# Performance work log

Measured on AMD Instinct MI355X. Metric: run time of the kernel, lower is better.

## Reference

```python
import jax, jax.numpy as jnp
import numpy as np

SCALING = 32.0 / 16.0  # alpha / r


def setup_inputs() -> dict:
    key = jax.random.key(0)
    k1, k2, k3, k4, k5 = jax.random.split(key, 5)
    B_, S, D_in, D_out, R = 4, 4096, 4096, 4096, 16
    x = jax.random.normal(k1, (B_, S, D_in), dtype=jnp.float32)
    W = jax.random.normal(k2, (D_in, D_out), dtype=jnp.float32) * 0.02
    b = jax.random.normal(k3, (D_out,), dtype=jnp.float32) * 0.02
    A = jax.random.normal(k4, (D_in, R), dtype=jnp.float32) * 0.02
    Bm = jax.random.normal(k5, (R, D_out), dtype=jnp.float32) * 0.02
    return {"x": x, "W": W, "b": b, "A": A, "B": Bm}


def reference(x, W, b, A, B):
    # base linear: y = x @ W + b  (torch Linear with weight W^T)
    base = jnp.einsum("bsd,de->bse", x, W) + b
    # low-rank update: x @ A @ B (associativity-exploiting; same math as x @ (A@B))
    lora = jnp.einsum("bsd,dr->bsr", x, A)
    lora = jnp.einsum("bsr,re->bse", lora, B)
    return base + lora * SCALING
```

## Files before the change

kernel.cpp:

```cpp
#include <hip/hip_runtime.h>

#define SCALE_LORA 2.0f
#define BM 256
#define BN 256
#define BKI 128

#define AS1 __attribute__((address_space(1)))
#define AS3 __attribute__((address_space(3)))

using f32x4  = __attribute__((ext_vector_type(4))) float;
using i32x4  = __attribute__((ext_vector_type(4))) int;
using i32x16 = __attribute__((ext_vector_type(16))) int;
using u16x8  = __attribute__((ext_vector_type(8))) unsigned short;

#define MFMAI8(a, b, c) __builtin_amdgcn_mfma_i32_32x32x32_i8((a), (b), (c), 0, 0, 0)

static __device__ __forceinline__ unsigned short f2bf_rne(float f) {
  unsigned int u = __builtin_bit_cast(unsigned int, f);
  u += 0x7FFFu + ((u >> 16) & 1u);
  return (unsigned short)(u >> 16);
}
static __device__ __forceinline__ float bf2f(unsigned short b) {
  unsigned int u = (unsigned int)b << 16;
  return __builtin_bit_cast(float, u);
}

__global__ void quant_x_kernel(const float* __restrict__ x,
                               signed char* __restrict__ xq,
                               float* __restrict__ sx, int K) {
  __shared__ float wmax[4];
  long row = blockIdx.x;
  const float* xr = x + row * (long)K;
  int t = threadIdx.x;
  f32x4 v[4];
  #pragma unroll
  for (int j = 0; j < 4; ++j)
    v[j] = *(const f32x4*)(xr + 4 * t + 1024 * j);
  float m = 0.f;
  #pragma unroll
  for (int j = 0; j < 4; ++j)
    #pragma unroll
    for (int e = 0; e < 4; ++e) m = fmaxf(m, fabsf(v[j][e]));
  #pragma unroll
  for (int off = 1; off < 64; off <<= 1)
    m = fmaxf(m, __shfl_xor(m, off));
  if ((t & 63) == 0) wmax[t >> 6] = m;
  __syncthreads();
  float rm = fmaxf(fmaxf(wmax[0], wmax[1]), fmaxf(wmax[2], wmax[3]));
  rm = fmaxf(rm, 1e-20f);
  float inv = 127.0f / rm;
  #pragma unroll
  for (int j = 0; j < 4; ++j) {
    int b0 = max(-127, min(127, (int)rintf(v[j][0] * inv)));
    int b1 = max(-127, min(127, (int)rintf(v[j][1] * inv)));
    int b2 = max(-127, min(127, (int)rintf(v[j][2] * inv)));
    int b3 = max(-127, min(127, (int)rintf(v[j][3] * inv)));
    unsigned int pk = (b0 & 255) | ((b1 & 255) << 8) | ((b2 & 255) << 16)
                      | ((unsigned)b3 << 24);
    *(unsigned int*)(xq + row * (long)K + 4 * t + 1024 * j) = pk;
  }
  if (t == 0) sx[row] = rm * (1.0f / 127.0f);
}

__global__ void build_wt_kernel(const float* __restrict__ W,
                                const float* __restrict__ A,
                                const float* __restrict__ Bmat,
                                unsigned short* __restrict__ WT,
                                int K, int N, int R) {
  __shared__ float Bs[16][64];
  __shared__ unsigned short Tt[64][66];
  int ntn = N >> 6;
  int kt = blockIdx.x / ntn, nt = blockIdx.x - kt * ntn;
  int k0 = kt << 6, n0 = nt << 6;
  int t = threadIdx.x;
  int tx = t & 63, ty = t >> 6;

  for (int i = t; i < R * 64; i += 256)
    Bs[i >> 6][i & 63] = Bmat[(long)(i >> 6) * N + n0 + (i & 63)];
  __syncthreads();

  for (int it = 0; it < 16; ++it) {
    int kl = (it << 2) + ty;
    long kg = k0 + kl;
    float w = W[kg * N + n0 + tx];
    const float* Ar = A + kg * R;
    float s = 0.f;
    for (int r = 0; r < R; ++r) s += Ar[r] * Bs[r][tx];
    Tt[kl][tx] = f2bf_rne(w + SCALE_LORA * s);
  }
  __syncthreads();

  for (int it = 0; it < 16; ++it) {
    int nn = (it << 2) + ty;
    WT[(long)(n0 + nn) * K + k0 + tx] = Tt[tx][nn];
  }
}

__global__ void quantize_wt_kernel(const unsigned short* __restrict__ WT,
                                   signed char* __restrict__ WTq,
                                   float* __restrict__ sw, int K) {
  __shared__ float wmax[4];
  long n = blockIdx.x;
  const unsigned short* wr = WT + n * (long)K;
  int t = threadIdx.x;
  u16x8 u0 = *(const u16x8*)(wr + 8 * t);
  u16x8 u1 = *(const u16x8*)(wr + 8 * t + 2048);
  float f0[8], f1[8];
  float m = 0.f;
  #pragma unroll
  for (int e = 0; e < 8; ++e) {
    f0[e] = bf2f(u0[e]); f1[e] = bf2f(u1[e]);
    m = fmaxf(m, fmaxf(fabsf(f0[e]), fabsf(f1[e])));
  }
  #pragma unroll
  for (int off = 1; off < 64; off <<= 1)
    m = fmaxf(m, __shfl_xor(m, off));
  if ((t & 63) == 0) wmax[t >> 6] = m;
  __syncthreads();
  float rm = fmaxf(fmaxf(wmax[0], wmax[1]), fmaxf(wmax[2], wmax[3]));
  rm = fmaxf(rm, 1e-20f);
  float inv = 127.0f / rm;
  unsigned long long p0 = 0, p1 = 0;
  #pragma unroll
  for (int e = 0; e < 8; ++e) {
    int q0 = max(-127, min(127, (int)rintf(f0[e] * inv)));
    int q1 = max(-127, min(127, (int)rintf(f1[e] * inv)));
    p0 |= (unsigned long long)(q0 & 255) << (8 * e);
    p1 |= (unsigned long long)(q1 & 255) << (8 * e);
  }
  *(unsigned long long*)(WTq + n * (long)K + 8 * t) = p0;
  *(unsigned long long*)(WTq + n * (long)K + 8 * t + 2048) = p1;
  if (t == 0) sw[n] = rm * (1.0f / 127.0f);
}

__global__ __launch_bounds__(512, 2) void gemm_kernel(
    const signed char* __restrict__ Xq,
    const signed char* __restrict__ WTq,
    const float* __restrict__ bias,
    const float* __restrict__ sx,
    const float* __restrict__ sw,
    float* __restrict__ out,
    int M, int N, int K)
{
  extern __shared__ char ldsc[];

  int nwg = gridDim.x;
  int bid = blockIdx.x;
  if ((nwg & 7) == 0) {
    int cpx = nwg >> 3;
    bid = (bid & 7) * cpx + (bid >> 3);
  }
  int ntn = N / BN;
  int tm = bid / ntn;
  int tn = bid - tm * ntn;
  const long m0 = (long)tm * BM;
  const long n0 = (long)tn * BN;

  int tid  = threadIdx.x;
  int lane = tid & 63;
  int wave = tid >> 6;
  int wr = wave >> 2;
  int wc = wave & 3;
  int l31 = lane & 31;
  int g   = lane >> 5;

  i32x16 acc[4][2] = {};

  int srcg = 16 * ((tid & 7) ^ ((tid >> 3) & 7));
  const signed char* aSrc = Xq + (m0 + (tid >> 3)) * (long)K + srcg;
  const signed char* bSrc = WTq + (n0 + (tid >> 3)) * (long)K + srcg;
  const int ldsByte = tid * 16;

  const int sw7 = l31 & 7;
  const int so0 = 16 * ((0 + g) ^ sw7);
  const int so1 = 16 * ((2 + g) ^ sw7);
  const int so2 = 16 * ((4 + g) ^ sw7);
  const int so3 = 16 * ((6 + g) ^ sw7);
  const int rowA = wr * 16384 + l31 * 128;
  const int rowB = wc * 8192  + l31 * 128;

  const int nt = K / BKI;

#define STGA(b, h, kt) do {                                                  \
    _Pragma("unroll")                                                        \
    for (int j_ = 0; j_ < 2; ++j_)                                           \
      __builtin_amdgcn_global_load_lds(                                      \
        (const AS1 void*)(aSrc + ((h)*128 + j_*64)*(long)K + (long)(kt)*BKI),\
        (AS3 void*)(ldsc + (b)*32768 + (h)*16384 + j_*8192 + ldsByte),       \
        16, 0, 0);                                                           \
  } while (0)
#define STGB(b, h, kt) do {                                                  \
    _Pragma("unroll")                                                        \
    for (int j_ = 0; j_ < 2; ++j_)                                           \
      __builtin_amdgcn_global_load_lds(                                      \
        (const AS1 void*)(bSrc + ((h)*128 + j_*64)*(long)K + (long)(kt)*BKI),\
        (AS3 void*)(ldsc + 65536 + (b)*32768 + (h)*16384 + j_*8192 +         \
                    ldsByte), 16, 0, 0);                                     \
  } while (0)

#define SBAR  __builtin_amdgcn_sched_barrier(0)
#define BAR   __builtin_amdgcn_s_barrier()
#define LGKM0 do { asm volatile("s_waitcnt lgkmcnt(0)" ::: "memory"); SBAR; } while (0)
#define LGKM8 do { asm volatile("s_waitcnt lgkmcnt(8)" ::: "memory"); } while (0)

#define RD_A(arr, fmB) do {                                                  \
    _Pragma("unroll")                                                        \
    for (int fi_ = 0; fi_ < 2; ++fi_) {                                      \
      const char* p_ = Ab_ + ((fmB) + fi_) * 4096;                           \
      arr[fi_][0] = *(const i32x4*)(p_ + so0);                               \
      arr[fi_][1] = *(const i32x4*)(p_ + so1);                               \
      arr[fi_][2] = *(const i32x4*)(p_ + so2);                               \
      arr[fi_][3] = *(const i32x4*)(p_ + so3);                               \
    }                                                                        \
  } while (0)
#define RD_B(arr, fnB) do {                                                  \
    const char* p_ = Bb_ + (fnB) * 4096;                                     \
    arr[0] = *(const i32x4*)(p_ + so0);                                      \
    arr[1] = *(const i32x4*)(p_ + so1);                                      \
    arr[2] = *(const i32x4*)(p_ + so2);                                      \
    arr[3] = *(const i32x4*)(p_ + so3);                                      \
  } while (0)
#define QUAD(aarr, barr, fmB, fn) do {                                       \
    __builtin_amdgcn_s_setprio(1);                                           \
    _Pragma("unroll")                                                        \
    for (int fi_ = 0; fi_ < 2; ++fi_)                                        \
      _Pragma("unroll")                                                      \
      for (int ks_ = 0; ks_ < 4; ++ks_)                                      \
        acc[(fmB)+fi_][fn] = MFMAI8(aarr[fi_][ks_], barr[ks_],               \
                                    acc[(fmB)+fi_][fn]);                     \
    __builtin_amdgcn_s_setprio(0);                                           \
  } while (0)

#define TILE4(B_, W1, S1, S2, S3, S4) do {                                   \
    asm volatile("s_waitcnt vmcnt(" W1 ")" ::: "memory");                    \
    BAR;                                                                     \
    const char* Ab_ = ldsc + (B_)*32768 + rowA;                              \
    const char* Bb_ = ldsc + 65536 + (B_)*32768 + rowB;                      \
    i32x4 af_[2][4], bl_[4], bh_[4], ag_[2][4];                              \
    RD_A(af_, 0);                                                            \
    RD_B(bl_, 0);                                                            \
    S1;                                                                      \
    LGKM8;                                                                   \
    SBAR; BAR; LGKM0;                                                        \
    QUAD(af_, bl_, 0, 0);                                                    \
    SBAR; BAR;                                                               \
    RD_B(bh_, 1);                                                            \
    S2;                                                                      \
    SBAR; BAR; LGKM0;                                                        \
    QUAD(af_, bh_, 0, 1);                                                    \
    SBAR; BAR;                                                               \
    RD_A(ag_, 2);                                                            \
    S3;                                                                      \
    SBAR; BAR; LGKM0;                                                        \
    QUAD(ag_, bl_, 2, 0);                                                    \
    SBAR; BAR;                                                               \
    S4;                                                                      \
    SBAR;                                                                    \
    QUAD(ag_, bh_, 2, 1);                                                    \
    SBAR;                                                                    \
  } while (0)

  STGB(0, 0, 0); STGA(0, 0, 0); STGB(0, 1, 0); STGA(0, 1, 0);
  STGB(1, 0, 1); STGA(1, 0, 1);

  const int npair = nt / 2;
  for (int i = 0; i < npair - 1; ++i) {
    int t2 = 2 * i;
    TILE4(0, "4", STGB(1,1,t2+1), STGA(1,1,t2+1), STGB(0,0,t2+2), STGA(0,0,t2+2));
    TILE4(1, "4", STGB(0,1,t2+2), STGA(0,1,t2+2), STGB(1,0,t2+3), STGA(1,0,t2+3));
  }
  TILE4(0, "4", STGB(1,1,nt-1), STGA(1,1,nt-1), , );
  TILE4(1, "0", , , , );

#undef TILE4
#undef QUAD
#undef RD_A
#undef RD_B
#undef STGA
#undef STGB

  #pragma unroll
  for (int fn = 0; fn < 2; ++fn) {
    long col = n0 + wc * 64 + fn * 32 + l31;
    float swc = sw[col];
    float bv = bias[col];
    #pragma unroll
    for (int fm = 0; fm < 4; ++fm) {
      long rbase = m0 + wr * 128 + fm * 32 + 4 * g;
      #pragma unroll
      for (int r = 0; r < 16; ++r) {
        long row = rbase + (r & 3) + 8 * (r >> 2);
        out[row * (long)N + col] = (float)acc[fm][fn][r] * sx[row] * swc + bv;
      }
    }
  }
}

extern "C" void kernel_launch(void* const* d_in, const int* in_sizes, int n_in,
                              void* d_out, int out_size, void* d_ws, size_t ws_size,
                              hipStream_t stream) {
  const float* x    = (const float*)d_in[0];
  const float* W    = (const float*)d_in[1];
  const float* b    = (const float*)d_in[2];
  const float* A    = (const float*)d_in[3];
  const float* Bm   = (const float*)d_in[4];

  const long D_out = in_sizes[2];
  const long D_in  = (long)in_sizes[1] / D_out;
  const long M     = (long)in_sizes[0] / D_in;
  const int  R     = (int)((long)in_sizes[3] / D_in);
  const int  K = (int)D_in, N = (int)D_out;

  char* wsc = (char*)d_ws;
  signed char*    xq  = (signed char*)wsc;
  unsigned short* wt  = (unsigned short*)(wsc + (size_t)M * K);
  signed char*    wtq = (signed char*)(wsc + (size_t)M * K + (size_t)N * K * 2);
  float* sx = (float*)(wsc + (size_t)M * K + (size_t)N * K * 3);
  float* sw = (float*)(wsc + (size_t)M * K + (size_t)N * K * 3 + (size_t)M * 4);

  quant_x_kernel<<<(int)M, 256, 0, stream>>>(x, xq, sx, K);
  build_wt_kernel<<<(K >> 6) * (N >> 6), 256, 0, stream>>>(W, A, Bm, wt, K, N, R);
  quantize_wt_kernel<<<N, 256, 0, stream>>>(wt, wtq, sw, K);

  int grid = (int)((M / BM) * ((long)N / BN));
  gemm_kernel<<<grid, 512, 128 * 1024, stream>>>(
      xq, wtq, b, sx, sw, (float*)d_out, (int)M, N, K);
}
```

Baseline: 446.3 us.

## Switch int8 GEMM main loop to 4-stage BK=64 pipeline with single barrier

Replaces the two-buffer, half-tile staged loop at K-step 128, which used many intra-tile barriers, with a four-buffer ring at K-step 64. Loads run three tiles ahead and each tile needs only one barrier. The LDS swizzle and row strides change to match the 64-byte rows. The aim is to cut barrier and synchronization overhead and to deepen prefetch. In exchange, the work per iteration halves and the bank-conflict behaviour of the new swizzle may differ.

```diff
diff --git a/kernel.cpp b/kernel.cpp
--- a/kernel.cpp
+++ b/kernel.cpp
@@ -3,7 +3,7 @@
 #define SCALE_LORA 2.0f
 #define BM 256
 #define BN 256
-#define BKI 128
+#define BKI 64
 
 #define AS1 __attribute__((address_space(1)))
 #define AS3 __attribute__((address_space(3)))
@@ -166,118 +166,92 @@
 
   i32x16 acc[4][2] = {};
 
-  int srcg = 16 * ((tid & 7) ^ ((tid >> 3) & 7));
-  const signed char* aSrc = Xq + (m0 + (tid >> 3)) * (long)K + srcg;
-  const signed char* bSrc = WTq + (n0 + (tid >> 3)) * (long)K + srcg;
+  int srccol = 16 * ((tid & 3) ^ ((tid >> 3) & 3));
+  const signed char* aSrc = Xq + (m0 + (tid >> 2)) * (long)K + srccol;
+  const signed char* bSrc = WTq + (n0 + (tid >> 2)) * (long)K + srccol;
   const int ldsByte = tid * 16;
 
-  const int sw7 = l31 & 7;
-  const int so0 = 16 * ((0 + g) ^ sw7);
-  const int so1 = 16 * ((2 + g) ^ sw7);
-  const int so2 = 16 * ((4 + g) ^ sw7);
-  const int so3 = 16 * ((6 + g) ^ sw7);
-  const int rowA = wr * 16384 + l31 * 128;
-  const int rowB = wc * 8192  + l31 * 128;
+  const int rsw = (l31 >> 1) & 3;
+  const int so0 = 16 * ((0 + g) ^ rsw);
+  const int so1 = 16 * ((2 + g) ^ rsw);
+  const int rowA = wr * 8192 + l31 * 64;
+  const int rowB = wc * 4096 + l31 * 64;
 
   const int nt = K / BKI;
 
-#define STGA(b, h, kt) do {                                                  \
+#define STAGEA(buf, kt) do {                                                 \
     _Pragma("unroll")                                                        \
     for (int j_ = 0; j_ < 2; ++j_)                                           \
       __builtin_amdgcn_global_load_lds(                                      \
-        (const AS1 void*)(aSrc + ((h)*128 + j_*64)*(long)K + (long)(kt)*BKI),\
-        (AS3 void*)(ldsc + (b)*32768 + (h)*16384 + j_*8192 + ldsByte),       \
+        (const AS1 void*)(aSrc + j_*128*(long)K + (long)(kt)*BKI),           \
+        (AS3 void*)(ldsc + (buf)*16384 + j_*8192 + ldsByte), 16, 0, 0);      \
+  } while (0)
+#define STAGEB(buf, kt) do {                                                 \
+    _Pragma("unroll")                                                        \
+    for (int j_ = 0; j_ < 2; ++j_)                                           \
+      __builtin_amdgcn_global_load_lds(                                      \
+        (const AS1 void*)(bSrc + j_*128*(long)K + (long)(kt)*BKI),           \
+        (AS3 void*)(ldsc + 65536 + (buf)*16384 + j_*8192 + ldsByte),         \
         16, 0, 0);                                                           \
   } while (0)
-#define STGB(b, h, kt) do {                                                  \
-    _Pragma("unroll")                                                        \
-    for (int j_ = 0; j_ < 2; ++j_)                                           \
-      __builtin_amdgcn_global_load_lds(                                      \
-        (const AS1 void*)(bSrc + ((h)*128 + j_*64)*(long)K + (long)(kt)*BKI),\
-        (AS3 void*)(ldsc + 65536 + (b)*32768 + (h)*16384 + j_*8192 +         \
-                    ldsByte), 16, 0, 0);                                     \
+
+#define SBAR  __builtin_amdgcn_sched_barrier(0)
+
+#define TILE(BUFI, VMSTR, STA, STB) do {                                     \
+    asm volatile("s_waitcnt vmcnt(" VMSTR ")" ::: "memory");                 \
+    __builtin_amdgcn_s_barrier();                                            \
+    SBAR;                                                                    \
+    const char* Ab_ = ldsc + (BUFI)*16384 + rowA;                            \
+    const char* Bb_ = ldsc + 65536 + (BUFI)*16384 + rowB;                    \
+    i32x4 a0_[4], a1_[4], b0_[2], b1_[2];                                    \
+    _Pragma("unroll")                                                        \
+    for (int fm_ = 0; fm_ < 4; ++fm_)                                        \
+      a0_[fm_] = *(const i32x4*)(Ab_ + fm_*2048 + so0);                      \
+    _Pragma("unroll")                                                        \
+    for (int fn_ = 0; fn_ < 2; ++fn_)                                        \
+      b0_[fn_] = *(const i32x4*)(Bb_ + fn_*2048 + so0);                      \
+    STA;                                                                     \
+    SBAR;                                                                    \
+    _Pragma("unroll")                                                        \
+    for (int fm_ = 0; fm_ < 4; ++fm_)                                        \
+      a1_[fm_] = *(const i32x4*)(Ab_ + fm_*2048 + so1);                      \
+    _Pragma("unroll")                                                        \
+    for (int fn_ = 0; fn_ < 2; ++fn_)                                        \
+      b1_[fn_] = *(const i32x4*)(Bb_ + fn_*2048 + so1);                      \
+    STB;                                                                     \
+    SBAR;                                                                    \
+    __builtin_amdgcn_s_setprio(1);                                           \
+    _Pragma("unroll")                                                        \
+    for (int fm_ = 0; fm_ < 4; ++fm_)                                        \
+      _Pragma("unroll")                                                      \
+      for (int fn_ = 0; fn_ < 2; ++fn_)                                      \
+        acc[fm_][fn_] = MFMAI8(a0_[fm_], b0_[fn_], acc[fm_][fn_]);           \
+    __builtin_amdgcn_s_setprio(0);                                           \
+    SBAR;                                                                    \
+    __builtin_amdgcn_s_setprio(1);                                           \
+    _Pragma("unroll")                                                        \
+    for (int fm_ = 0; fm_ < 4; ++fm_)                                        \
+      _Pragma("unroll")                                                      \
+      for (int fn_ = 0; fn_ < 2; ++fn_)                                      \
+        acc[fm_][fn_] = MFMAI8(a1_[fm_], b1_[fn_], acc[fm_][fn_]);           \
+    __builtin_amdgcn_s_setprio(0);                                           \
+    SBAR;                                                                    \
   } while (0)
 
-#define SBAR  __builtin_amdgcn_sched_barrier(0)
-#define BAR   __builtin_amdgcn_s_barrier()
-#define LGKM0 do { asm volatile("s_waitcnt lgkmcnt(0)" ::: "memory"); SBAR; } while (0)
-#define LGKM8 do { asm volatile("s_waitcnt lgkmcnt(8)" ::: "memory"); } while (0)
-
-#define RD_A(arr, fmB) do {                                                  \
-    _Pragma("unroll")                                                        \
-    for (int fi_ = 0; fi_ < 2; ++fi_) {                                      \
-      const char* p_ = Ab_ + ((fmB) + fi_) * 4096;                           \
-      arr[fi_][0] = *(const i32x4*)(p_ + so0);                               \
-      arr[fi_][1] = *(const i32x4*)(p_ + so1);                               \
-      arr[fi_][2] = *(const i32x4*)(p_ + so2);                               \
-      arr[fi_][3] = *(const i32x4*)(p_ + so3);                               \
-    }                                                                        \
-  } while (0)
-#define RD_B(arr, fnB) do {                                                  \
-    const char* p_ = Bb_ + (fnB) * 4096;                                     \
-    arr[0] = *(const i32x4*)(p_ + so0);                                      \
-    arr[1] = *(const i32x4*)(p_ + so1);                                      \
-    arr[2] = *(const i32x4*)(p_ + so2);                                      \
-    arr[3] = *(const i32x4*)(p_ + so3);                                      \
-  } while (0)
-#define QUAD(aarr, barr, fmB, fn) do {                                       \
-    __builtin_amdgcn_s_setprio(1);                                           \
-    _Pragma("unroll")                                                        \
-    for (int fi_ = 0; fi_ < 2; ++fi_)                                        \
-      _Pragma("unroll")                                                      \
-      for (int ks_ = 0; ks_ < 4; ++ks_)                                      \
-        acc[(fmB)+fi_][fn] = MFMAI8(aarr[fi_][ks_], barr[ks_],               \
-                                    acc[(fmB)+fi_][fn]);                     \
-    __builtin_amdgcn_s_setprio(0);                                           \
-  } while (0)
-
-#define TILE4(B_, W1, S1, S2, S3, S4) do {                                   \
-    asm volatile("s_waitcnt vmcnt(" W1 ")" ::: "memory");                    \
-    BAR;                                                                     \
-    const char* Ab_ = ldsc + (B_)*32768 + rowA;                              \
-    const char* Bb_ = ldsc + 65536 + (B_)*32768 + rowB;                      \
-    i32x4 af_[2][4], bl_[4], bh_[4], ag_[2][4];                              \
-    RD_A(af_, 0);                                                            \
-    RD_B(bl_, 0);                                                            \
-    S1;                                                                      \
-    LGKM8;                                                                   \
-    SBAR; BAR; LGKM0;                                                        \
-    QUAD(af_, bl_, 0, 0);                                                    \
-    SBAR; BAR;                                                               \
-    RD_B(bh_, 1);                                                            \
-    S2;                                                                      \
-    SBAR; BAR; LGKM0;                                                        \
-    QUAD(af_, bh_, 0, 1);                                                    \
-    SBAR; BAR;                                                               \
-    RD_A(ag_, 2);                                                            \
-    S3;                                                                      \
-    SBAR; BAR; LGKM0;                                                        \
-    QUAD(ag_, bl_, 2, 0);                                                    \
-    SBAR; BAR;                                                               \
-    S4;                                                                      \
-    SBAR;                                                                    \
-    QUAD(ag_, bh_, 2, 1);                                                    \
-    SBAR;                                                                    \
-  } while (0)
-
-  STGB(0, 0, 0); STGA(0, 0, 0); STGB(0, 1, 0); STGA(0, 1, 0);
-  STGB(1, 0, 1); STGA(1, 0, 1);
-
-  const int npair = nt / 2;
-  for (int i = 0; i < npair - 1; ++i) {
-    int t2 = 2 * i;
-    TILE4(0, "4", STGB(1,1,t2+1), STGA(1,1,t2+1), STGB(0,0,t2+2), STGA(0,0,t2+2));
-    TILE4(1, "4", STGB(0,1,t2+2), STGA(0,1,t2+2), STGB(1,0,t2+3), STGA(1,0,t2+3));
-  }
-  TILE4(0, "4", STGB(1,1,nt-1), STGA(1,1,nt-1), , );
-  TILE4(1, "0", , , , );
-
-#undef TILE4
-#undef QUAD
-#undef RD_A
-#undef RD_B
-#undef STGA
-#undef STGB
+  STAGEA(0, 0); STAGEB(0, 0);
+  STAGEA(1, 1); STAGEB(1, 1);
+  STAGEA(2, 2); STAGEB(2, 2);
+
+  for (int t = 0; t < nt - 3; ++t) {
+    TILE(t & 3, "8", STAGEA((t + 3) & 3, t + 3), STAGEB((t + 3) & 3, t + 3));
+  }
+  TILE((nt - 3) & 3, "8", , );
+  TILE((nt - 2) & 3, "4", , );
+  TILE((nt - 1) & 3, "0", , );
+
+#undef TILE
+#undef STAGEA
+#undef STAGEB
 
   #pragma unroll
   for (int fn = 0; fn < 2; ++fn) {
```

After: 461.7 us. 1.03x slower.
